# Kernel tuning notes

Hardware: AMD Instinct MI355X
Metric: run time of the kernel (lower is better)

The kernel has to match this reference:

```python
import jax, jax.numpy as jnp
import numpy as np

N, F, H, C, E, L = 100000, 512, 64, 40, 1600000, 6


def setup_inputs() -> dict:
    key = jax.random.key(0)
    ks = jax.random.split(key, 2 * L + 4)
    x = jax.random.normal(ks[0], (N, F), dtype=jnp.float32)
    edge_index = jax.random.randint(ks[1], (2, E), 0, N, dtype=jnp.int32)
    inp = {"x": x, "edge_index": edge_index}
    in_dims = [F + H * i for i in range(L)]  # 512, 576, ..., 832 (dense concat)
    for i in range(L):
        inp[f"W{i}"] = jax.random.normal(ks[2 + i], (in_dims[i], H), dtype=jnp.float32) / np.sqrt(in_dims[i]).astype(np.float32)
        inp[f"b{i}"] = jnp.zeros((H,), dtype=jnp.float32)
    jk_dim = in_dims[-1] + H  # 896 = num_features + 6*H
    inp["Wlin"] = jax.random.normal(ks[2 + L], (jk_dim, C), dtype=jnp.float32) / np.sqrt(jk_dim).astype(np.float32)
    inp["blin"] = jnp.zeros((C,), dtype=jnp.float32)
    return inp


def _gcn_norm(edge_index, num_nodes, dtype):
    # Add self loops, compute symmetric normalization deg^-1/2 * deg^-1/2
    loop = jnp.arange(num_nodes, dtype=edge_index.dtype)
    row = jnp.concatenate([edge_index[0], loop])  # source
    col = jnp.concatenate([edge_index[1], loop])  # target
    deg = jax.ops.segment_sum(jnp.ones_like(col, dtype=dtype), col, num_segments=num_nodes)
    dinv = jnp.where(deg > 0, jax.lax.rsqrt(jnp.maximum(deg, 1.0)), 0.0)
    norm = dinv[row] * dinv[col]  # [E + N]
    return row, col, norm


def reference(x, edge_index, W0, b0, W1, b1, W2, b2, W3, b3, W4, b4, W5, b5, Wlin, blin):
    Ws = [W0, W1, W2, W3, W4, W5]
    bs = [b0, b1, b2, b3, b4, b5]
    n = x.shape[0]
    row, col, norm = _gcn_norm(edge_index, n, x.dtype)

    xs = [x]
    for W, b in zip(Ws, bs):
        inp = jnp.concatenate(xs, axis=1)          # dense (DenseNet-style) concat
        lin = inp @ W                               # [n, H] transform before propagate
        msg = lin[row] * norm[:, None]              # gather + edge weight
        agg = jax.ops.segment_sum(msg, col, num_segments=n)  # scatter-add aggregate
        h = jax.nn.relu(agg + b)                    # GCNConv bias, then ReLU (dropout = eval mode)
        xs.append(h)

    hcat = jnp.concatenate(xs, axis=1)              # JumpingKnowledge('cat')
    logits = hcat @ Wlin + blin
    return jax.nn.log_softmax(logits, axis=1)
```

## Files before the change

### kernel.cpp

```cpp
#include <hip/hip_runtime.h>
#include <hip/hip_bf16.h>

#define HH 64
#define XDIM 896
#define FF 512
#define LL 6
#define CC 40
#define CBSZ 512
#define SLACK 10240
#define NSEG 13

typedef __bf16 bf16x8 __attribute__((ext_vector_type(8)));
typedef float f32x4 __attribute__((ext_vector_type(4)));

__device__ __forceinline__ unsigned short f2bf(float f){
  union{float f; unsigned int u;} v; v.f=f; unsigned int u=v.u;
  return (unsigned short)((u + 0x7fffu + ((u>>16)&1u))>>16);
}
__device__ __forceinline__ float bf2f(unsigned short u){
  union{unsigned int u; float f;} v; v.u = ((unsigned int)u)<<16; return v.f;
}
__device__ __forceinline__ float u2f(unsigned u){
  union{unsigned u; float f;} v; v.u=u; return v.f;
}

struct PrepP {
  const float* x; const int* ei;
  unsigned short* X; unsigned short* lin;
  int* bcur; unsigned* tmp;
  const float* W[NSEG]; unsigned short* dst[NSEG];
  int nt[NSEG], nc[NSEG], tst[NSEG], tbs[NSEG], kbase[NSEG];
  int off[NSEG+1];
  int N, E, CH, NB, WB;
};

__global__ void __launch_bounds__(256) k_prep(PrepP P){
  __shared__ int hist[256];
  __shared__ int run[256];
  int t=threadIdx.x, b=blockIdx.x;
  if (b < 256){
    int E=P.E;
    int lo=b*P.CH, hi=lo+P.CH; if (hi>E) hi=E;
    for (int i=t;i<P.NB;i+=256) hist[i]=0;
    __syncthreads();
    for (int i=lo+t;i<hi;i+=256) atomicAdd(&hist[P.ei[E+i]>>9], 1);
    __syncthreads();
    for (int i=t;i<P.NB;i+=256) run[i]=i*SLACK+atomicAdd(&P.bcur[i], hist[i]);
    __syncthreads();
    for (int i=lo+t;i<hi;i+=256){
      int r=P.ei[i], c=P.ei[E+i];
      int pos=atomicAdd(&run[c>>9],1);
      P.tmp[pos]=((unsigned)r<<9)|(unsigned)(c&(CBSZ-1));
    }
  } else if (b < 256+P.WB){
    int idx=(b-256)*256+t;
    if (idx < P.off[NSEG]){
      int seg=0;
      while (idx>=P.off[seg+1]) ++seg;
      int li=idx-P.off[seg];
      int j=li&7, ln=(li>>3)&63, rem2=li>>9;
      int ntile=P.nt[seg], ncols=P.nc[seg];
      int nt_=rem2%ntile, kb=rem2/ntile;
      int k=P.kbase[seg]+kb*32+(ln>>4)*8+j;
      int c=nt_*16+(ln&15);
      float v=(c<ncols)? P.W[seg][(size_t)k*ncols+c] : 0.f;
      int di = ((kb*P.tst[seg] + P.tbs[seg] + nt_)*64 + ln)*8 + j;
      P.dst[seg][di]=f2bf(v);
    }
  } else {
    int i=(b-256-P.WB)*256+t;
    if (i<32) ((unsigned*)(P.lin+(size_t)P.N*64))[i]=0u;
    int total=P.N*(FF/4);
    if (i<total){
      int row=i/(FF/4), c4=(i%(FF/4))*4;
      float4 v=*(const float4*)(P.x+(size_t)row*FF+c4);
      ushort4 o; o.x=f2bf(v.x); o.y=f2bf(v.y); o.z=f2bf(v.z); o.w=f2bf(v.w);
      *(ushort4*)(P.X+(size_t)row*XDIM+c4)=o;
    }
  }
}

__global__ void __launch_bounds__(1024) k_build(const unsigned* __restrict__ tmp,
                                                const int* __restrict__ bcur,
                                                int* __restrict__ offsS, int* __restrict__ offsE,
                                                float* __restrict__ dinv,
                                                int* __restrict__ esrc, int N){
  __shared__ int cnt[CBSZ];
  __shared__ int run[CBSZ];
  int t=threadIdx.x, b=blockIdx.x;
  int n0=b*CBSZ;
  int nloc=N-n0; if (nloc>CBSZ) nloc=CBSZ;
  int wbase=b*SLACK;
  int wend=wbase + bcur[b];
  if (t<CBSZ) cnt[t]=0;
  __syncthreads();
  for (int i=wbase+t; i<wend; i+=1024) atomicAdd(&cnt[tmp[i]&(CBSZ-1u)],1);
  __syncthreads();
  int v = (t<CBSZ)? cnt[t] : 0;
  if (t<CBSZ) run[t]=v;
  __syncthreads();
  for (int o=1;o<CBSZ;o<<=1){
    int xx = (t<CBSZ && t>=o)? run[t-o] : 0;
    __syncthreads();
    if (t<CBSZ) run[t]+=xx;
    __syncthreads();
  }
  if (t<nloc){
    int s = wbase + (run[t]-v);
    offsS[n0+t]=s;
    offsE[n0+t]=s+v;
    dinv[n0+t]=rsqrtf((float)(v+1));
    run[t]=s;
  }
  __syncthreads();
  for (int i=wbase+t; i<wend; i+=1024){
    unsigned vv=tmp[i];
    int pos=atomicAdd(&run[vv&(CBSZ-1u)],1);
    esrc[pos]=(int)(vv>>9);
  }
}

struct GBP {
  const unsigned short* X; const unsigned short* WfBig;
  const float* dinv;
  unsigned short* pl[6];
  float* pF;
  int N;
};

__global__ void __launch_bounds__(256) k_gbig(GBP P){
  int t=threadIdx.x, lane=t&63, wid=t>>6;
  int tb = wid*7;
  long row0 = (long)blockIdx.x*32;
  int arow=lane&15, kgrp=lane>>4;
  long r0=row0+arow;    if (r0>(long)P.N-1) r0=P.N-1;
  long r1=row0+16+arow; if (r1>(long)P.N-1) r1=P.N-1;
  const unsigned short* ap0 = P.X + (size_t)r0*XDIM + kgrp*8;
  const unsigned short* ap1 = P.X + (size_t)r1*XDIM + kgrp*8;
  const unsigned short* bbase = P.WfBig + (size_t)tb*512 + lane*8;
  f32x4 acc0[7], acc1[7];
  #pragma unroll
  for (int i=0;i<7;i++){ f32x4 z={0.f,0.f,0.f,0.f}; acc0[i]=z; acc1[i]=z; }
  for (int kb=0;kb<16;++kb){
    bf16x8 a0=*(const bf16x8*)(ap0+(size_t)kb*32);
    bf16x8 a1=*(const bf16x8*)(ap1+(size_t)kb*32);
    const unsigned short* bp = bbase + (size_t)kb*28*512;
    #pragma unroll
    for (int tt=0;tt<7;++tt){
      bf16x8 b=*(const bf16x8*)(bp + tt*512);
      acc0[tt]=__builtin_amdgcn_mfma_f32_16x16x32_bf16(a0,b,acc0[tt],0,0,0);
      acc1[tt]=__builtin_amdgcn_mfma_f32_16x16x32_bf16(a1,b,acc1[tt],0,0,0);
    }
  }
  #pragma unroll
  for (int tt=0;tt<7;++tt){
    int tg = tb+tt;
    if (tg >= 27) continue;
    #pragma unroll
    for (int j=0;j<4;++j){
      long rr=row0+kgrp*4+j;
      long rr1=rr+16;
      if (tg<24){
        int li=tg>>2, tloc=tg&3;
        if (rr<P.N){
          float s = (li==0) ? P.dinv[rr] : 1.f;
          P.pl[li][(size_t)rr*64 + tloc*16 + arow] = f2bf(acc0[tt][j]*s);
        }
        if (rr1<P.N){
          float s = (li==0) ? P.dinv[rr1] : 1.f;
          P.pl[li][(size_t)rr1*64 + tloc*16 + arow] = f2bf(acc1[tt][j]*s);
        }
      } else {
        int c=(tg-24)*16+arow;
        if (c<CC){
          if (rr<P.N)  P.pF[(size_t)rr*CC+c]=acc0[tt][j];
          if (rr1<P.N) P.pF[(size_t)rr1*CC+c]=acc1[tt][j];
        }
      }
    }
  }
}

__global__ void __launch_bounds__(256) k_gemmH(const unsigned short* __restrict__ X,
                                               const unsigned short* __restrict__ WfH,
                                               const unsigned short* __restrict__ part,
                                               const float* __restrict__ dinv,
                                               unsigned short* __restrict__ lin,
                                               int N, int nkb2){
  int lane = threadIdx.x & 63, wid = threadIdx.x >> 6;
  long row0 = (long)blockIdx.x*128 + wid*32;
  int arow = lane & 15, kgrp = lane >> 4;
  long r0 = row0 + arow;      if (r0 > (long)N-1) r0 = N-1;
  long r1 = row0 + 16 + arow; if (r1 > (long)N-1) r1 = N-1;
  const unsigned short* ap0 = X + (size_t)r0*XDIM + FF + kgrp*8;
  const unsigned short* ap1 = X + (size_t)r1*XDIM + FF + kgrp*8;
  const unsigned short* bptr = WfH + lane*8;
  f32x4 acc00={0.f,0.f,0.f,0.f}, acc01=acc00, acc02=acc00, acc03=acc00;
  f32x4 acc10=acc00, acc11=acc00, acc12=acc00, acc13=acc00;
  for (int kb=0; kb<nkb2; ++kb){
    bf16x8 a0 = *(const bf16x8*)(ap0 + (size_t)kb*32);
    bf16x8 a1 = *(const bf16x8*)(ap1 + (size_t)kb*32);
    const unsigned short* bp = bptr + (size_t)kb*2048;
    bf16x8 b0=*(const bf16x8*)bp, b1=*(const bf16x8*)(bp+512),
           b2=*(const bf16x8*)(bp+1024), b3=*(const bf16x8*)(bp+1536);
    acc00=__builtin_amdgcn_mfma_f32_16x16x32_bf16(a0,b0,acc00,0,0,0);
    acc10=__builtin_amdgcn_mfma_f32_16x16x32_bf16(a1,b0,acc10,0,0,0);
    acc01=__builtin_amdgcn_mfma_f32_16x16x32_bf16(a0,b1,acc01,0,0,0);
    acc11=__builtin_amdgcn_mfma_f32_16x16x32_bf16(a1,b1,acc11,0,0,0);
    acc02=__builtin_amdgcn_mfma_f32_16x16x32_bf16(a0,b2,acc02,0,0,0);
    acc12=__builtin_amdgcn_mfma_f32_16x16x32_bf16(a1,b2,acc12,0,0,0);
    acc03=__builtin_amdgcn_mfma_f32_16x16x32_bf16(a0,b3,acc03,0,0,0);
    acc13=__builtin_amdgcn_mfma_f32_16x16x32_bf16(a1,b3,acc13,0,0,0);
  }
  for (int j=0;j<4;++j){
    long rr = row0 + kgrp*4 + j;
    if (rr < N){
      float dv = dinv[rr];
      const unsigned short* pp = part + (size_t)rr*64 + arow;
      unsigned short* lp = lin + (size_t)rr*64 + arow;
      lp[0]  = f2bf((acc00[j]+bf2f(pp[0]))*dv);
      lp[16] = f2bf((acc01[j]+bf2f(pp[16]))*dv);
      lp[32] = f2bf((acc02[j]+bf2f(pp[32]))*dv);
      lp[48] = f2bf((acc03[j]+bf2f(pp[48]))*dv);
    }
    long rr1 = rr + 16;
    if (rr1 < N){
      float dv = dinv[rr1];
      const unsigned short* pp = part + (size_t)rr1*64 + arow;
      unsigned short* lp = lin + (size_t)rr1*64 + arow;
      lp[0]  = f2bf((acc10[j]+bf2f(pp[0]))*dv);
      lp[16] = f2bf((acc11[j]+bf2f(pp[16]))*dv);
      lp[32] = f2bf((acc12[j]+bf2f(pp[32]))*dv);
      lp[48] = f2bf((acc13[j]+bf2f(pp[48]))*dv);
    }
  }
}

__global__ void __launch_bounds__(256) k_agg(const unsigned short* __restrict__ lin,
                                             const int* __restrict__ offsS,
                                             const int* __restrict__ offsE,
                                             const int* __restrict__ esrc,
                                             const float* __restrict__ dinv,
                                             const float* __restrict__ bias,
                                             unsigned short* __restrict__ X,
                                             int colbase, int N){
  int lane = threadIdx.x & 63, wid = threadIdx.x >> 6;
  int n = blockIdx.x*4 + wid;
  if (n >= N) return;
  int sub = lane >> 4;
  int fq  = lane & 15;
  const unsigned short* lq = lin + fq*4;
  float a0=0.f, a1=0.f, a2=0.f, a3=0.f;
  int s = offsS[n], e = offsE[n];
  int base = s;
  for (; base + 32 <= e; base += 32){
    #pragma unroll
    for (int k=0;k<8;++k){
      int sx = esrc[base + 4*k + sub];
      uint2 v = *(const uint2*)(lq + (size_t)sx*64);
      a0 += u2f(v.x<<16); a1 += u2f(v.x&0xffff0000u);
      a2 += u2f(v.y<<16); a3 += u2f(v.y&0xffff0000u);
    }
  }
  if (base < e){
    int rem = e - base;
    if (rem > 16){
      #pragma unroll
      for (int k=0;k<8;++k){
        int idx = 4*k + sub;
        int sx = esrc[base + idx];
        sx = (idx < rem) ? sx : (int)N;
        uint2 v = *(const uint2*)(lq + (size_t)sx*64);
        a0 += u2f(v.x<<16); a1 += u2f(v.x&0xffff0000u);
        a2 += u2f(v.y<<16); a3 += u2f(v.y&0xffff0000u);
      }
    } else {
      #pragma unroll
      for (int k=0;k<4;++k){
        int idx = 4*k + sub;
        int sx = esrc[base + idx];
        sx = (idx < rem) ? sx : (int)N;
        uint2 v = *(const uint2*)(lq + (size_t)sx*64);
        a0 += u2f(v.x<<16); a1 += u2f(v.x&0xffff0000u);
        a2 += u2f(v.y<<16); a3 += u2f(v.y&0xffff0000u);
      }
    }
  }
  a0 += __shfl_xor(a0,16,64); a0 += __shfl_xor(a0,32,64);
  a1 += __shfl_xor(a1,16,64); a1 += __shfl_xor(a1,32,64);
  a2 += __shfl_xor(a2,16,64); a2 += __shfl_xor(a2,32,64);
  a3 += __shfl_xor(a3,16,64); a3 += __shfl_xor(a3,32,64);
  uint2 vs = *(const uint2*)(lq + (size_t)n*64);
  a0 += u2f(vs.x<<16); a1 += u2f(vs.x&0xffff0000u);
  a2 += u2f(vs.y<<16); a3 += u2f(vs.y&0xffff0000u);
  float dv = dinv[n];
  float4 b4 = *(const float4*)(bias + fq*4);
  float h0 = fmaxf(a0*dv + b4.x, 0.f);
  float h1 = fmaxf(a1*dv + b4.y, 0.f);
  float h2 = fmaxf(a2*dv + b4.z, 0.f);
  float h3 = fmaxf(a3*dv + b4.w, 0.f);
  if (sub == 0){
    ushort4 o; o.x=f2bf(h0); o.y=f2bf(h1); o.z=f2bf(h2); o.w=f2bf(h3);
    *(ushort4*)(X + (size_t)n*XDIM + colbase + fq*4) = o;
  }
}

__global__ void __launch_bounds__(256) k_final(const unsigned short* __restrict__ X,
                                               const unsigned short* __restrict__ Wf,
                                               const float* __restrict__ pF,
                                               const float* __restrict__ blin,
                                               float* __restrict__ out, int N){
  int lane=threadIdx.x&63, wid=threadIdx.x>>6;
  long row0=(long)blockIdx.x*64 + wid*16;
  int c0=lane&15, g=lane>>4;
  long r=row0+c0; if (r > (long)N-1) r = N-1;
  const unsigned short* aptr = X + (size_t)r*XDIM + FF + g*8;
  const unsigned short* bptr = Wf + lane*8;
  f32x4 acc0={0.f,0.f,0.f,0.f}, acc1=acc0, acc2=acc0;
  const int nkb = (XDIM-FF)/32;
  for (int kb=0;kb<nkb;++kb){
    bf16x8 a=*(const bf16x8*)(aptr+(size_t)kb*32);
    const unsigned short* bp = bptr + (size_t)kb*1536;
    bf16x8 b0=*(const bf16x8*)bp, b1=*(const bf16x8*)(bp+512), b2=*(const bf16x8*)(bp+1024);
    acc0=__builtin_amdgcn_mfma_f32_16x16x32_bf16(a,b0,acc0,0,0,0);
    acc1=__builtin_amdgcn_mfma_f32_16x16x32_bf16(a,b1,acc1,0,0,0);
    acc2=__builtin_amdgcn_mfma_f32_16x16x32_bf16(a,b2,acc2,0,0,0);
  }
  float bl0 = blin[c0], bl1 = blin[16+c0];
  bool v2ok = (c0 < 8);
  float bl2 = v2ok ? blin[32+c0] : 0.f;
  for (int j=0;j<4;++j){
    long rr = row0 + g*4 + j;
    long rrc = rr < N ? rr : (long)N-1;
    const float* pp = pF + (size_t)rrc*CC;
    float v0 = acc0[j]+bl0+pp[c0], v1 = acc1[j]+bl1+pp[16+c0];
    float v2 = v2ok ? (acc2[j]+bl2+pp[32+c0]) : -1e30f;
    float m = fmaxf(fmaxf(v0,v1),v2);
    m = fmaxf(m, __shfl_xor(m,1,64));
    m = fmaxf(m, __shfl_xor(m,2,64));
    m = fmaxf(m, __shfl_xor(m,4,64));
    m = fmaxf(m, __shfl_xor(m,8,64));
    float sEx = expf(v0-m)+expf(v1-m)+(v2ok?expf(v2-m):0.f);
    sEx += __shfl_xor(sEx,1,64);
    sEx += __shfl_xor(sEx,2,64);
    sEx += __shfl_xor(sEx,4,64);
    sEx += __shfl_xor(sEx,8,64);
    float lse = m + logf(sEx);
    if (rr < N){
      out[(size_t)rr*CC + c0]      = v0 - lse;
      out[(size_t)rr*CC + 16 + c0] = v1 - lse;
      if (v2ok) out[(size_t)rr*CC + 32 + c0] = v2 - lse;
    }
  }
}

extern "C" void kernel_launch(void* const* d_in, const int* in_sizes, int n_in,
                              void* d_out, int out_size, void* d_ws, size_t ws_size,
                              hipStream_t stream){
  const float* x = (const float*)d_in[0];
  const int* ei = (const int*)d_in[1];
  const float* Wl[LL]; const float* bl[LL];
  for (int i=0;i<LL;i++){ Wl[i]=(const float*)d_in[2+2*i]; bl[i]=(const float*)d_in[3+2*i]; }
  const float* Wlin = (const float*)d_in[2+2*LL];
  const float* blin = (const float*)d_in[3+2*LL];
  float* out = (float*)d_out;
  const int N = in_sizes[0]/FF;
  const int E = in_sizes[1]/2;
  const int NB = (N+CBSZ-1)/CBSZ;

  char* p = (char*)d_ws;
  auto alloc = [&](size_t bb)->char*{ char* r=p; p += (bb+255)&~(size_t)255; return r; };
  unsigned short* X   = (unsigned short*)alloc((size_t)N*XDIM*2);
  unsigned short* lin = (unsigned short*)alloc((size_t)(N+1)*64*2);
  unsigned* tmp = (unsigned*)lin;
  unsigned short* WfBig  = (unsigned short*)alloc((size_t)16*28*512*2);
  unsigned short* WfH[LL];
  for (int i=1;i<LL;i++) WfH[i]=(unsigned short*)alloc((size_t)(2*i)*4*512*2);
  unsigned short* WfLinH = (unsigned short*)alloc((size_t)12*3*512*2);
  unsigned short* part[LL];
  for (int i=1;i<LL;i++) part[i]=(unsigned short*)alloc((size_t)N*64*2);
  float* pF    = (float*)alloc((size_t)N*CC*4);
  float* dinv  = (float*)alloc((size_t)N*4);
  int* offsS   = (int*)alloc((size_t)N*4);
  int* offsE   = (int*)alloc((size_t)N*4);
  int* bcur    = (int*)alloc((size_t)NB*4);
  int* esrc    = (int*)alloc(((size_t)NB*SLACK+64)*4);

  PrepP P;
  P.x=x; P.ei=ei; P.X=X; P.lin=lin; P.bcur=bcur; P.tmp=tmp;
  int off=0, sg=0;
  for (int i=0;i<LL;i++){
    P.W[sg]=Wl[i]; P.dst[sg]=WfBig; P.nt[sg]=4; P.nc[sg]=HH;
    P.tst[sg]=28; P.tbs[sg]=4*i; P.kbase[sg]=0;
    P.off[sg]=off; off += 16*4*512; ++sg;
  }
  P.W[sg]=Wlin; P.dst[sg]=WfBig; P.nt[sg]=3; P.nc[sg]=CC;
  P.tst[sg]=28; P.tbs[sg]=24; P.kbase[sg]=0;
  P.off[sg]=off; off += 16*3*512; ++sg;
  for (int i=1;i<LL;i++){
    P.W[sg]=Wl[i]; P.dst[sg]=WfH[i]; P.nt[sg]=4; P.nc[sg]=HH;
    P.tst[sg]=4; P.tbs[sg]=0; P.kbase[sg]=FF;
    P.off[sg]=off; off += (2*i)*4*512; ++sg;
  }
  P.W[sg]=Wlin; P.dst[sg]=WfLinH; P.nt[sg]=3; P.nc[sg]=CC;
  P.tst[sg]=3; P.tbs[sg]=0; P.kbase[sg]=FF;
  P.off[sg]=off; off += 12*3*512; ++sg;
  P.off[sg]=off;
  P.N=N; P.E=E; P.CH=(E+255)/256; P.NB=NB; P.WB=(off+255)/256;
  int XB=(N*(FF/4)+255)/256;

  hipMemsetAsync(bcur, 0, (size_t)NB*4, stream);
  k_prep <<<256 + P.WB + XB, 256, 0, stream>>>(P);
  k_build<<<NB, 1024, 0, stream>>>(tmp, bcur, offsS, offsE, dinv, esrc, N);

  GBP G;
  G.X=X; G.WfBig=WfBig; G.dinv=dinv;
  G.pl[0]=lin;
  for (int i=1;i<LL;i++) G.pl[i]=part[i];
  G.pF=pF; G.N=N;
  k_gbig<<<(N+31)/32, 256, 0, stream>>>(G);

  int gb = (N+127)/128;
  int ab = (N+3)/4;
  for (int i=0;i<LL;i++){
    if (i>0) k_gemmH<<<gb,256,0,stream>>>(X, WfH[i], part[i], dinv, lin, N, 2*i);
    k_agg<<<ab,256,0,stream>>>(lin, offsS, offsE, esrc, dinv, bl[i], X, FF+HH*i, N);
  }
  k_final<<<(N+63)/64,256,0,stream>>>(X, WfLinH, pF, blin, out, N);
}
```

Before: 591.5 us.

## Stage A tiles in LDS with async global_load_lds double buffering in k_gbig

Restructures the big GEMM so each block covers 128 rows and one of four column groups, with A tiles loaded asynchronously into an XOR-swizzled, double-buffered LDS buffer through global_load_lds while MFMAs run on the previous tile. B fragments are preloaded into registers per k-step. The aim is to overlap global-memory latency with compute and share A rows across waves. In exchange, each row tile of A is now loaded by four different blocks, and the loop adds a barrier per k-step.

```diff
diff --git a/kernel.cpp b/kernel.cpp
--- a/kernel.cpp
+++ b/kernel.cpp
@@ -23,6 +23,10 @@
 __device__ __forceinline__ float u2f(unsigned u){
   union{unsigned u; float f;} v; v.u=u; return v.f;
 }
+
+#define GLD16(gsrc, ldsdst) \
+  __builtin_amdgcn_global_load_lds((const __attribute__((address_space(1))) unsigned int*)(gsrc), \
+                                   (__attribute__((address_space(3))) unsigned int*)(ldsdst), 16, 0, 0)
 
 struct PrepP {
   const float* x; const int* ei;
@@ -129,29 +133,53 @@
 };
 
 __global__ void __launch_bounds__(256) k_gbig(GBP P){
-  int t=threadIdx.x, lane=t&63, wid=t>>6;
-  int tb = wid*7;
-  long row0 = (long)blockIdx.x*32;
+  __shared__ unsigned short Abuf[2][128*32];
+  int t=threadIdx.x, lane=t&63, wv=t>>6;
+  int bid = blockIdx.x;
+  int cg = bid & 3;
+  long rb = (long)(bid>>2)*128;
+  int tb = cg*7;
   int arow=lane&15, kgrp=lane>>4;
-  long r0=row0+arow;    if (r0>(long)P.N-1) r0=P.N-1;
-  long r1=row0+16+arow; if (r1>(long)P.N-1) r1=P.N-1;
-  const unsigned short* ap0 = P.X + (size_t)r0*XDIM + kgrp*8;
-  const unsigned short* ap1 = P.X + (size_t)r1*XDIM + kgrp*8;
-  const unsigned short* bbase = P.WfBig + (size_t)tb*512 + lane*8;
+
+  int srow0 = wv*32 + (lane>>2);
+  int srow1 = srow0 + 16;
+  int scb   = 16*((lane&3) ^ (srow0&3));
+  long gr0 = rb + srow0; if (gr0 > (long)P.N-1) gr0 = P.N-1;
+  long gr1 = rb + srow1; if (gr1 > (long)P.N-1) gr1 = P.N-1;
+  const char* gs0 = (const char*)P.X + gr0*(XDIM*2) + scb;
+  const char* gs1 = (const char*)P.X + gr1*(XDIM*2) + scb;
+
   f32x4 acc0[7], acc1[7];
   #pragma unroll
   for (int i=0;i<7;i++){ f32x4 z={0.f,0.f,0.f,0.f}; acc0[i]=z; acc1[i]=z; }
+
+  GLD16(gs0, &Abuf[0][(wv*2+0)*512]);
+  GLD16(gs1, &Abuf[0][(wv*2+1)*512]);
+  __syncthreads();
+
+  int kofs = 16*(kgrp ^ (arow&3));
   for (int kb=0;kb<16;++kb){
-    bf16x8 a0=*(const bf16x8*)(ap0+(size_t)kb*32);
-    bf16x8 a1=*(const bf16x8*)(ap1+(size_t)kb*32);
-    const unsigned short* bp = bbase + (size_t)kb*28*512;
+    int cur = kb&1;
+    if (kb<15){
+      GLD16(gs0 + (kb+1)*64, &Abuf[cur^1][(wv*2+0)*512]);
+      GLD16(gs1 + (kb+1)*64, &Abuf[cur^1][(wv*2+1)*512]);
+    }
+    const unsigned short* bp = P.WfBig + ((size_t)kb*28 + tb)*512 + lane*8;
+    bf16x8 bv[7];
+    #pragma unroll
+    for (int tt=0;tt<7;++tt) bv[tt]=*(const bf16x8*)(bp + (size_t)tt*512);
+    int lr0 = wv*32 + arow;
+    bf16x8 a0 = *(const bf16x8*)((const char*)&Abuf[cur][0] + lr0*64 + kofs);
+    bf16x8 a1 = *(const bf16x8*)((const char*)&Abuf[cur][0] + (lr0+16)*64 + kofs);
     #pragma unroll
     for (int tt=0;tt<7;++tt){
-      bf16x8 b=*(const bf16x8*)(bp + tt*512);
-      acc0[tt]=__builtin_amdgcn_mfma_f32_16x16x32_bf16(a0,b,acc0[tt],0,0,0);
-      acc1[tt]=__builtin_amdgcn_mfma_f32_16x16x32_bf16(a1,b,acc1[tt],0,0,0);
-    }
-  }
+      acc0[tt]=__builtin_amdgcn_mfma_f32_16x16x32_bf16(a0,bv[tt],acc0[tt],0,0,0);
+      acc1[tt]=__builtin_amdgcn_mfma_f32_16x16x32_bf16(a1,bv[tt],acc1[tt],0,0,0);
+    }
+    __syncthreads();
+  }
+
+  long row0 = rb + wv*32;
   #pragma unroll
   for (int tt=0;tt<7;++tt){
     int tg = tb+tt;
@@ -418,7 +446,8 @@
   G.pl[0]=lin;
   for (int i=1;i<LL;i++) G.pl[i]=part[i];
   G.pF=pF; G.N=N;
-  k_gbig<<<(N+31)/32, 256, 0, stream>>>(G);
+  int rbks = (N+127)/128;
+  k_gbig<<<rbks*4, 256, 0, stream>>>(G);
 
   int gb = (N+127)/128;
   int ab = (N+3)/4;
```

Measured after the change: 594.7 us. Within noise of the previous version (+0.5%).
